# Optimization experiments

Measured on AMD Instinct MI355X. Metric: run time of the kernel, lower is better.

Reference implementation:

```python
import jax, jax.numpy as jnp
import numpy as np

N_NODES = 50000
N_EDGES = 800000
DIMS = [128, 128, 128, 64]  # in, hid1, hid2, out
EPS = 1e-12


def setup_inputs() -> dict:
    key = jax.random.key(0)
    ks = jax.random.split(key, 32)
    inp = {
        "x": jax.random.normal(ks[0], (N_NODES, DIMS[0]), dtype=jnp.float32),
        "edge_src": jax.random.randint(ks[1], (N_EDGES,), 0, N_NODES),
        "edge_dst": jax.random.randint(ks[2], (N_EDGES,), 0, N_NODES),
    }
    k = 3
    for l in range(3):
        din, dout = DIMS[l], DIMS[l + 1]
        s_in = 1.0 / np.sqrt(din)
        inp[f"Wp{l+1}"] = jax.random.uniform(ks[k], (din, din), jnp.float32, -s_in, s_in); k += 1
        inp[f"bp{l+1}"] = jax.random.uniform(ks[k], (din,), jnp.float32, -s_in, s_in); k += 1
        inp[f"Ws{l+1}"] = jax.random.uniform(ks[k], (din, dout), jnp.float32, -s_in, s_in); k += 1
        inp[f"Wn{l+1}"] = jax.random.uniform(ks[k], (din, dout), jnp.float32, -s_in, s_in); k += 1
        inp[f"b{l+1}"] = jnp.zeros((dout,), jnp.float32); k += 1
    return inp


def _sage_pool_layer(x, src, dst, Wp, bp, Ws, Wn, b):
    # per-edge: relu(fc_pool(x_src)); [E, din]
    m = jax.nn.relu(x[src] @ Wp + bp)
    # max-pool over in-neighbors of each dst node; [N, din]
    pooled = jax.ops.segment_max(m, dst, num_segments=x.shape[0])
    deg = jax.ops.segment_sum(jnp.ones((dst.shape[0],), x.dtype), dst,
                              num_segments=x.shape[0])
    pooled = jnp.where(deg[:, None] > 0, pooled, 0.0)  # zero-degree -> 0 (DGL)
    return x @ Ws + pooled @ Wn + b


def _l2norm_relu(h):
    n = jnp.sqrt(jnp.sum(h * h, axis=1, keepdims=True))
    return jax.nn.relu(h / jnp.maximum(n, EPS))


def reference(x, edge_src, edge_dst,
              Wp1, bp1, Ws1, Wn1, b1,
              Wp2, bp2, Ws2, Wn2, b2,
              Wp3, bp3, Ws3, Wn3, b3):
    h = _l2norm_relu(_sage_pool_layer(x, edge_src, edge_dst, Wp1, bp1, Ws1, Wn1, b1))
    h = _l2norm_relu(_sage_pool_layer(h, edge_src, edge_dst, Wp2, bp2, Ws2, Wn2, b2))
    h = _l2norm_relu(_sage_pool_layer(h, edge_src, edge_dst, Wp3, bp3, Ws3, Wn3, b3))
    return h
```

## Files before the change

### kernel.cpp

```cpp
#include <hip/hip_runtime.h>
#include <math.h>

#define N_NODES 50000
#define N_EDGES 800000
#define CAP 64
#define RANGES 8
#define NODES_PER_RANGE 6250
#define GEMMB 782
#define CHUNKS (N_EDGES / 256)
#define CPB 8
#define BPR ((CHUNKS + CPB - 1) / CPB)
#define CSRB (BPR * RANGES)
#define LROW 136

typedef __attribute__((ext_vector_type(8))) short short8;
typedef __attribute__((ext_vector_type(4))) float f32x4;

__device__ __forceinline__ unsigned short f2bf(float f) {
    unsigned int u = __float_as_uint(f);
    return (unsigned short)((u + 0x7FFFu + ((u >> 16) & 1u)) >> 16);
}

template <bool F32>
__device__ __forceinline__ short8 loadA(const void* A, int off) {
    short8 r;
    if (F32) {
        const float* p = (const float*)A + off;
        float4 f0 = *(const float4*)p;
        float4 f1 = *(const float4*)(p + 4);
        r[0] = (short)f2bf(f0.x); r[1] = (short)f2bf(f0.y);
        r[2] = (short)f2bf(f0.z); r[3] = (short)f2bf(f0.w);
        r[4] = (short)f2bf(f1.x); r[5] = (short)f2bf(f1.y);
        r[6] = (short)f2bf(f1.z); r[7] = (short)f2bf(f1.w);
    } else {
        r = *(const short8*)((const unsigned short*)A + off);
    }
    return r;
}

__device__ __forceinline__ void issue8(short8 (&v)[8],
    const unsigned short* a0, const unsigned short* a1) {
    asm volatile(
        "global_load_dwordx4 %0, %8, off\n\t"
        "global_load_dwordx4 %1, %8, off offset:16\n\t"
        "global_load_dwordx4 %2, %8, off offset:32\n\t"
        "global_load_dwordx4 %3, %8, off offset:48\n\t"
        "global_load_dwordx4 %4, %9, off\n\t"
        "global_load_dwordx4 %5, %9, off offset:16\n\t"
        "global_load_dwordx4 %6, %9, off offset:32\n\t"
        "global_load_dwordx4 %7, %9, off offset:48"
        : "=&v"(v[0]), "=&v"(v[1]), "=&v"(v[2]), "=&v"(v[3]),
          "=&v"(v[4]), "=&v"(v[5]), "=&v"(v[6]), "=&v"(v[7])
        : "v"(a0), "v"(a1));
}

__device__ __forceinline__ void wait_vm8(short8 (&v)[8]) {
    asm volatile("s_waitcnt vmcnt(8)"
        : "+v"(v[0]), "+v"(v[1]), "+v"(v[2]), "+v"(v[3]),
          "+v"(v[4]), "+v"(v[5]), "+v"(v[6]), "+v"(v[7]) :: "memory");
}

__device__ __forceinline__ void wait_vm0(short8 (&v)[8]) {
    asm volatile("s_waitcnt vmcnt(0)"
        : "+v"(v[0]), "+v"(v[1]), "+v"(v[2]), "+v"(v[3]),
          "+v"(v[4]), "+v"(v[5]), "+v"(v[6]), "+v"(v[7]) :: "memory");
}

__device__ __forceinline__ void consume8(short8 (&p)[4], const short8 (&v)[8]) {
    p[0] = __builtin_elementwise_max(p[0], v[0]);
    p[1] = __builtin_elementwise_max(p[1], v[1]);
    p[2] = __builtin_elementwise_max(p[2], v[2]);
    p[3] = __builtin_elementwise_max(p[3], v[3]);
    p[0] = __builtin_elementwise_max(p[0], v[4]);
    p[1] = __builtin_elementwise_max(p[1], v[5]);
    p[2] = __builtin_elementwise_max(p[2], v[6]);
    p[3] = __builtin_elementwise_max(p[3], v[7]);
}

struct WDescs { const float* W[9]; int N[9]; };

__global__ __launch_bounds__(256) void prep_kernel(
    WDescs wd, unsigned short* __restrict__ Wpk, int* __restrict__ deg)
{
    const int nthr = gridDim.x * 256;
    const int tid = blockIdx.x * 256 + threadIdx.x;
    for (int id = tid; id < 9 * 16384; id += nthr) {
        int mi = id >> 14;
        int loc = id & 16383;
        int N = wd.N[mi];
        if (loc < 128 * N) {
            int c = loc / (N * 32);
            int n = (loc - c * N * 32) >> 5;
            int k = c * 32 + (loc & 31);
            Wpk[mi * 16384 + loc] = f2bf(wd.W[mi][k * N + n]);
        }
    }
    for (int i = tid; i < N_NODES; i += nthr) deg[i] = 0;
}

__global__ __launch_bounds__(256) void mix_kernel(
    const int* __restrict__ esrc, const int* __restrict__ edst,
    int* __restrict__ deg, unsigned short* __restrict__ csr16,
    const float* __restrict__ x, const unsigned short* __restrict__ Wp1,
    const float* __restrict__ bp1, unsigned short* __restrict__ Y)
{
    if (blockIdx.x >= GEMMB) {
        const int b = blockIdx.x - GEMMB;
        const int range = b & (RANGES - 1);
        const int cbase = (b >> 3) * CPB;
        const int lo = range * NODES_PER_RANGE;
        int d[CPB], s[CPB];
        #pragma unroll
        for (int i = 0; i < CPB; ++i) {
            const int c = cbase + i;
            const int e = c * 256 + threadIdx.x;
            const bool ok = (c < CHUNKS);
            d[i] = ok ? edst[e] : -1;
            s[i] = ok ? esrc[e] : 0;
        }
        #pragma unroll
        for (int i = 0; i < CPB; ++i) {
            if ((unsigned)(d[i] - lo) < (unsigned)NODES_PER_RANGE) {
                int r = atomicAdd(&deg[d[i]], 1);
                if (r < CAP) csr16[(d[i] << 6) + r] = (unsigned short)s[i];
            }
        }
        return;
    }
    const int lane = threadIdx.x & 63;
    const int wv = threadIdx.x >> 6;
    const int cl = lane & 15;
    const int quad = lane >> 4;
    const int rowBase = blockIdx.x * 64 + wv * 16;
    const int ar = min(rowBase + cl, N_NODES - 1);
    const int bLane = cl * 32 + quad * 8;

    f32x4 acc[8];
    #pragma unroll
    for (int t = 0; t < 8; ++t) acc[t] = (f32x4){0.f, 0.f, 0.f, 0.f};

    #pragma unroll
    for (int c = 0; c < 4; ++c) {
        short8 af = loadA<true>(x, ar * 128 + c * 32 + quad * 8);
        const unsigned short* Bc = Wp1 + c * 4096 + bLane;
        #pragma unroll
        for (int t = 0; t < 8; ++t) {
            short8 bf = *(const short8*)(Bc + t * 512);
            acc[t] = __builtin_amdgcn_mfma_f32_16x16x32_bf16(af, bf, acc[t], 0, 0, 0);
        }
    }
    const int row0 = rowBase + quad * 4;
    #pragma unroll
    for (int t = 0; t < 8; ++t) {
        float bc = bp1[t * 16 + cl];
        #pragma unroll
        for (int g = 0; g < 4; ++g) {
            int r = row0 + g;
            if (r < N_NODES)
                Y[r * 128 + t * 16 + cl] = f2bf(fmaxf(acc[t][g] + bc, 0.0f));
        }
    }
}

template <bool A0F32, bool LAST>
__global__ __launch_bounds__(256) void fused_kernel(
    const void* __restrict__ A0,
    const unsigned short* __restrict__ Yl,
    const int* __restrict__ deg,
    const unsigned short* __restrict__ csr16,
    const unsigned short* __restrict__ B0, const unsigned short* __restrict__ B1,
    const float* __restrict__ bias,
    unsigned short* __restrict__ outH, float* __restrict__ outF,
    const unsigned short* __restrict__ Bnext, const float* __restrict__ bnext,
    unsigned short* __restrict__ Yout)
{
    constexpr int NT = LAST ? 4 : 8;
    constexpr int N = NT * 16;
    __shared__ unsigned short lds[4][16 * LROW];

    const int lane = threadIdx.x & 63;
    const int wv = threadIdx.x >> 6;
    const int cl = lane & 15;
    const int quad = lane >> 4;
    const int nodeBase = blockIdx.x * 64 + wv * 16;
    unsigned short* plw = &lds[wv][0];

    {
        const int n16 = lane >> 2;
        const int g   = lane & 3;
        const int node = nodeBase + n16;
        const int nodeC = min(node, N_NODES - 1);
        const int myDeg = (node < N_NODES) ? min(deg[node], CAP) : 0;
        const unsigned short* csrn = csr16 + (nodeC << 6);
        const unsigned short* yg = Yl + g * 32;

        short8 p[4];
        p[0] = (short8){0,0,0,0,0,0,0,0};
        p[1] = p[0]; p[2] = p[0]; p[3] = p[0];

        if (myDeg > 0) {
            unsigned int idxw[16];
            *(uint4*)(idxw +  0) = *(const uint4*)(csrn +  0);
            *(uint4*)(idxw +  4) = *(const uint4*)(csrn +  8);
            *(uint4*)(idxw +  8) = *(const uint4*)(csrn + 16);
            *(uint4*)(idxw + 12) = *(const uint4*)(csrn + 24);
            const int s0 = (int)(idxw[0] & 0xFFFFu);

            auto eaddr = [&](int jj) -> const unsigned short* {
                int sj = (jj & 1) ? (int)(idxw[jj >> 1] >> 16)
                                  : (int)(idxw[jj >> 1] & 0xFFFFu);
                sj = (jj < myDeg) ? sj : s0;
                return yg + (sj << 7);
            };

            short8 va[8], vb[8];
            issue8(va, eaddr(0),  eaddr(1));
            issue8(vb, eaddr(2),  eaddr(3));
            wait_vm8(va); consume8(p, va); issue8(va, eaddr(4),  eaddr(5));
            wait_vm8(vb); consume8(p, vb); issue8(vb, eaddr(6),  eaddr(7));
            wait_vm8(va); consume8(p, va); issue8(va, eaddr(8),  eaddr(9));
            wait_vm8(vb); consume8(p, vb); issue8(vb, eaddr(10), eaddr(11));
            wait_vm8(va); consume8(p, va); issue8(va, eaddr(12), eaddr(13));
            wait_vm8(vb); consume8(p, vb); issue8(vb, eaddr(14), eaddr(15));
            if (myDeg > 16) {
                wait_vm8(va); consume8(p, va); issue8(va, eaddr(16), eaddr(17));
                wait_vm8(vb); consume8(p, vb); issue8(vb, eaddr(18), eaddr(19));
                wait_vm8(va); consume8(p, va); issue8(va, eaddr(20), eaddr(21));
                wait_vm8(vb); consume8(p, vb); issue8(vb, eaddr(22), eaddr(23));
                wait_vm8(va); consume8(p, va); issue8(va, eaddr(24), eaddr(25));
                wait_vm8(vb); consume8(p, vb); issue8(vb, eaddr(26), eaddr(27));
                wait_vm8(va); consume8(p, va); issue8(va, eaddr(28), eaddr(29));
                wait_vm8(vb); consume8(p, vb); issue8(vb, eaddr(30), eaddr(31));
            }
            wait_vm8(va); consume8(p, va);
            wait_vm0(vb); consume8(p, vb);

            for (int k = 32; k < myDeg; ++k) {
                const short8* r = (const short8*)(yg + ((int)csrn[k] << 7));
                p[0] = __builtin_elementwise_max(p[0], r[0]);
                p[1] = __builtin_elementwise_max(p[1], r[1]);
                p[2] = __builtin_elementwise_max(p[2], r[2]);
                p[3] = __builtin_elementwise_max(p[3], r[3]);
            }
        }
        unsigned short* pw = plw + n16 * LROW + g * 32;
        *(short8*)(pw)      = p[0];
        *(short8*)(pw + 8)  = p[1];
        *(short8*)(pw + 16) = p[2];
        *(short8*)(pw + 24) = p[3];
    }

    const int ar = min(nodeBase + cl, N_NODES - 1);
    const int aBase = ar * 128 + quad * 8;
    const int fBase = cl * LROW + quad * 8;
    const int bLane = cl * 32 + quad * 8;

    f32x4 acc[NT];
    #pragma unroll
    for (int t = 0; t < NT; ++t) acc[t] = (f32x4){0.f, 0.f, 0.f, 0.f};

    #pragma unroll
    for (int c = 0; c < 4; ++c) {
        short8 a0 = loadA<A0F32>(A0, aBase + c * 32);
        short8 a1 = *(const short8*)(plw + fBase + c * 32);
        const unsigned short* B0c = B0 + c * (N * 32) + bLane;
        const unsigned short* B1c = B1 + c * (N * 32) + bLane;
        #pragma unroll
        for (int t = 0; t < NT; ++t) {
            short8 bf = *(const short8*)(B0c + t * 512);
            acc[t] = __builtin_amdgcn_mfma_f32_16x16x32_bf16(a0, bf, acc[t], 0, 0, 0);
        }
        #pragma unroll
        for (int t = 0; t < NT; ++t) {
            short8 bf = *(const short8*)(B1c + t * 512);
            acc[t] = __builtin_amdgcn_mfma_f32_16x16x32_bf16(a1, bf, acc[t], 0, 0, 0);
        }
    }

    #pragma unroll
    for (int t = 0; t < NT; ++t) {
        float bc = bias[t * 16 + cl];
        #pragma unroll
        for (int g = 0; g < 4; ++g) acc[t][g] += bc;
    }

    float inv[4];
    #pragma unroll
    for (int g = 0; g < 4; ++g) {
        float s = 0.f;
        #pragma unroll
        for (int t = 0; t < NT; ++t) s += acc[t][g] * acc[t][g];
        s += __shfl_xor(s, 1, 64);
        s += __shfl_xor(s, 2, 64);
        s += __shfl_xor(s, 4, 64);
        s += __shfl_xor(s, 8, 64);
        inv[g] = 1.0f / fmaxf(sqrtf(s), 1e-12f);
    }

    const int row0 = nodeBase + quad * 4;

    if (LAST) {
        #pragma unroll
        for (int t = 0; t < NT; ++t)
            #pragma unroll
            for (int g = 0; g < 4; ++g) {
                int r = row0 + g;
                if (r < N_NODES)
                    outF[r * N + t * 16 + cl] = fmaxf(acc[t][g] * inv[g], 0.0f);
            }
        return;
    }

    #pragma unroll
    for (int t = 0; t < NT; ++t)
        #pragma unroll
        for (int g = 0; g < 4; ++g) {
            int r = row0 + g;
            unsigned short h = f2bf(fmaxf(acc[t][g] * inv[g], 0.0f));
            if (r < N_NODES) outH[r * 128 + t * 16 + cl] = h;
            plw[(quad * 4 + g) * LROW + t * 16 + cl] = h;
        }

    f32x4 ya[8];
    #pragma unroll
    for (int t = 0; t < 8; ++t) ya[t] = (f32x4){0.f, 0.f, 0.f, 0.f};
    #pragma unroll
    for (int c = 0; c < 4; ++c) {
        short8 af = *(const short8*)(plw + cl * LROW + c * 32 + quad * 8);
        const unsigned short* Bc = Bnext + c * 4096 + bLane;
        #pragma unroll
        for (int t = 0; t < 8; ++t) {
            short8 bf = *(const short8*)(Bc + t * 512);
            ya[t] = __builtin_amdgcn_mfma_f32_16x16x32_bf16(af, bf, ya[t], 0, 0, 0);
        }
    }
    #pragma unroll
    for (int t = 0; t < 8; ++t) {
        float bc = bnext[t * 16 + cl];
        #pragma unroll
        for (int g = 0; g < 4; ++g) {
            int r = row0 + g;
            if (r < N_NODES)
                Yout[r * 128 + t * 16 + cl] = f2bf(fmaxf(ya[t][g] + bc, 0.0f));
        }
    }
}

extern "C" void kernel_launch(void* const* d_in, const int* in_sizes, int n_in,
                              void* d_out, int out_size, void* d_ws, size_t ws_size,
                              hipStream_t stream) {
    const float* x    = (const float*)d_in[0];
    const int*   esrc = (const int*)d_in[1];
    const int*   edst = (const int*)d_in[2];
    const float* Wp[3], *bp[3], *Ws[3], *Wn[3], *bb[3];
    for (int l = 0; l < 3; ++l) {
        Wp[l] = (const float*)d_in[3 + 5 * l];
        bp[l] = (const float*)d_in[4 + 5 * l];
        Ws[l] = (const float*)d_in[5 + 5 * l];
        Wn[l] = (const float*)d_in[6 + 5 * l];
        bb[l] = (const float*)d_in[7 + 5 * l];
    }

    const int NF = N_NODES * 128;
    unsigned short* YA  = (unsigned short*)d_ws;
    unsigned short* YB  = YA + NF;
    unsigned short* PL  = YB + NF;
    unsigned short* H1  = PL + NF;
    unsigned short* H2  = H1 + NF;
    unsigned short* Wpk = H2 + NF;
    int* deg = (int*)(Wpk + 9 * 16384);
    unsigned short* csr16 = (unsigned short*)(deg + N_NODES);

    auto WH = [&](int i) { return Wpk + i * 16384; };

    WDescs wd;
    wd.W[0] = Wp[0]; wd.N[0] = 128;
    wd.W[1] = Ws[0]; wd.N[1] = 128;
    wd.W[2] = Wn[0]; wd.N[2] = 128;
    wd.W[3] = Wp[1]; wd.N[3] = 128;
    wd.W[4] = Ws[1]; wd.N[4] = 128;
    wd.W[5] = Wn[1]; wd.N[5] = 128;
    wd.W[6] = Wp[2]; wd.N[6] = 128;
    wd.W[7] = Ws[2]; wd.N[7] = 64;
    wd.W[8] = Wn[2]; wd.N[8] = 64;

    prep_kernel<<<576, 256, 0, stream>>>(wd, Wpk, deg);
    mix_kernel<<<GEMMB + CSRB, 256, 0, stream>>>(esrc, edst, deg, csr16,
                                                 x, WH(0), bp[0], YA);
    fused_kernel<true, false><<<GEMMB, 256, 0, stream>>>(
        x, YA, deg, csr16, WH(1), WH(2), bb[0], H1, nullptr, WH(3), bp[1], YB);
    fused_kernel<false, false><<<GEMMB, 256, 0, stream>>>(
        H1, YB, deg, csr16, WH(4), WH(5), bb[1], H2, nullptr, WH(6), bp[2], YA);
    fused_kernel<false, true><<<GEMMB, 256, 0, stream>>>(
        H2, YA, deg, csr16, WH(7), WH(8), bb[2], nullptr, (float*)d_out,
        nullptr, nullptr, nullptr);
}
```

Before: 331.4 us.

## Fuse all stages into one cooperative persistent kernel with grid syncs

Merges the prep, mix and three fused layer kernels into a single cooperative mega kernel that loops over tasks and separates stages with grid-wide barriers, falling back to separate launches when cooperative launch or occupancy is unavailable. This removes per-kernel launch gaps and the tail between stages. In exchange, grid syncs and thread fences cost time, register pressure is shared across all stage code paths, and the mix stage's CSR blocks must now be looped over by the 782 resident blocks.

After: 336.9 us. About the same (+1.7%).

```diff
diff --git a/kernel.cpp b/kernel.cpp
--- a/kernel.cpp
+++ b/kernel.cpp
@@ -1,5 +1,8 @@
 #include <hip/hip_runtime.h>
+#include <hip/hip_cooperative_groups.h>
 #include <math.h>
+
+namespace cg = cooperative_groups;
 
 #define N_NODES 50000
 #define N_EDGES 800000
@@ -79,8 +82,8 @@
 
 struct WDescs { const float* W[9]; int N[9]; };
 
-__global__ __launch_bounds__(256) void prep_kernel(
-    WDescs wd, unsigned short* __restrict__ Wpk, int* __restrict__ deg)
+__device__ __forceinline__ void do_prep(const WDescs& wd,
+    unsigned short* __restrict__ Wpk, int* __restrict__ deg)
 {
     const int nthr = gridDim.x * 256;
     const int tid = blockIdx.x * 256 + threadIdx.x;
@@ -98,14 +101,14 @@
     for (int i = tid; i < N_NODES; i += nthr) deg[i] = 0;
 }
 
-__global__ __launch_bounds__(256) void mix_kernel(
+__device__ __forceinline__ void do_mix(int task,
     const int* __restrict__ esrc, const int* __restrict__ edst,
     int* __restrict__ deg, unsigned short* __restrict__ csr16,
     const float* __restrict__ x, const unsigned short* __restrict__ Wp1,
     const float* __restrict__ bp1, unsigned short* __restrict__ Y)
 {
-    if (blockIdx.x >= GEMMB) {
-        const int b = blockIdx.x - GEMMB;
+    if (task >= GEMMB) {
+        const int b = task - GEMMB;
         const int range = b & (RANGES - 1);
         const int cbase = (b >> 3) * CPB;
         const int lo = range * NODES_PER_RANGE;
@@ -131,7 +134,7 @@
     const int wv = threadIdx.x >> 6;
     const int cl = lane & 15;
     const int quad = lane >> 4;
-    const int rowBase = blockIdx.x * 64 + wv * 16;
+    const int rowBase = task * 64 + wv * 16;
     const int ar = min(rowBase + cl, N_NODES - 1);
     const int bLane = cl * 32 + quad * 8;
 
@@ -163,7 +166,7 @@
 }
 
 template <bool A0F32, bool LAST>
-__global__ __launch_bounds__(256) void fused_kernel(
+__device__ __forceinline__ void do_fused(int task, unsigned short* ldsAll,
     const void* __restrict__ A0,
     const unsigned short* __restrict__ Yl,
     const int* __restrict__ deg,
@@ -176,14 +179,13 @@
 {
     constexpr int NT = LAST ? 4 : 8;
     constexpr int N = NT * 16;
-    __shared__ unsigned short lds[4][16 * LROW];
 
     const int lane = threadIdx.x & 63;
     const int wv = threadIdx.x >> 6;
     const int cl = lane & 15;
     const int quad = lane >> 4;
-    const int nodeBase = blockIdx.x * 64 + wv * 16;
-    unsigned short* plw = &lds[wv][0];
+    const int nodeBase = task * 64 + wv * 16;
+    unsigned short* plw = ldsAll + wv * (16 * LROW);
 
     {
         const int n16 = lane >> 2;
@@ -346,6 +348,81 @@
     }
 }
 
+struct MegaArgs {
+    const float* x;
+    const int* esrc; const int* edst;
+    WDescs wd;
+    unsigned short *YA, *YB, *H1, *H2, *Wpk;
+    int* deg; unsigned short* csr16;
+    const float *bp1, *bp2, *bp3;
+    const float *b1, *b2, *b3;
+    float* outF;
+};
+
+__device__ __forceinline__ void gsync(cg::grid_group& g) {
+    __threadfence();
+    g.sync();
+    __threadfence();
+}
+
+__global__ __launch_bounds__(256) void mega_kernel(MegaArgs a)
+{
+    cg::grid_group grid = cg::this_grid();
+    __shared__ unsigned short lds[4][16 * LROW];
+    unsigned short* ldsAll = &lds[0][0];
+    const int G = gridDim.x;
+    auto WHd = [&](int i) { return a.Wpk + i * 16384; };
+
+    do_prep(a.wd, a.Wpk, a.deg);
+    gsync(grid);
+    for (int t = blockIdx.x; t < GEMMB + CSRB; t += G)
+        do_mix(t, a.esrc, a.edst, a.deg, a.csr16, a.x, WHd(0), a.bp1, a.YA);
+    gsync(grid);
+    for (int t = blockIdx.x; t < GEMMB; t += G)
+        do_fused<true, false>(t, ldsAll, a.x, a.YA, a.deg, a.csr16,
+            WHd(1), WHd(2), a.b1, a.H1, nullptr, WHd(3), a.bp2, a.YB);
+    gsync(grid);
+    for (int t = blockIdx.x; t < GEMMB; t += G)
+        do_fused<false, false>(t, ldsAll, a.H1, a.YB, a.deg, a.csr16,
+            WHd(4), WHd(5), a.b2, a.H2, nullptr, WHd(6), a.bp3, a.YA);
+    gsync(grid);
+    for (int t = blockIdx.x; t < GEMMB; t += G)
+        do_fused<false, true>(t, ldsAll, a.H2, a.YA, a.deg, a.csr16,
+            WHd(7), WHd(8), a.b3, nullptr, a.outF, nullptr, nullptr, nullptr);
+}
+
+__global__ __launch_bounds__(256) void prep_kernel(
+    WDescs wd, unsigned short* __restrict__ Wpk, int* __restrict__ deg)
+{
+    do_prep(wd, Wpk, deg);
+}
+
+__global__ __launch_bounds__(256) void mix_kernel(
+    const int* __restrict__ esrc, const int* __restrict__ edst,
+    int* __restrict__ deg, unsigned short* __restrict__ csr16,
+    const float* __restrict__ x, const unsigned short* __restrict__ Wp1,
+    const float* __restrict__ bp1, unsigned short* __restrict__ Y)
+{
+    do_mix(blockIdx.x, esrc, edst, deg, csr16, x, Wp1, bp1, Y);
+}
+
+template <bool A0F32, bool LAST>
+__global__ __launch_bounds__(256) void fused_kernel(
+    const void* __restrict__ A0,
+    const unsigned short* __restrict__ Yl,
+    const int* __restrict__ deg,
+    const unsigned short* __restrict__ csr16,
+    const unsigned short* __restrict__ B0, const unsigned short* __restrict__ B1,
+    const float* __restrict__ bias,
+    unsigned short* __restrict__ outH, float* __restrict__ outF,
+    const unsigned short* __restrict__ Bnext, const float* __restrict__ bnext,
+    unsigned short* __restrict__ Yout)
+{
+    __shared__ unsigned short lds[4][16 * LROW];
+    do_fused<A0F32, LAST>(blockIdx.x, &lds[0][0], A0, Yl, deg, csr16,
+                          B0, B1, bias, outH, outF, Bnext, bnext, Yout);
+}
+
 extern "C" void kernel_launch(void* const* d_in, const int* in_sizes, int n_in,
                               void* d_out, int out_size, void* d_ws, size_t ws_size,
                               hipStream_t stream) {
@@ -384,6 +461,35 @@
     wd.W[7] = Ws[2]; wd.N[7] = 64;
     wd.W[8] = Wn[2]; wd.N[8] = 64;
 
+    static int s_mega = -1;
+    if (s_mega < 0) {
+        int coop = 0;
+        hipDeviceGetAttribute(&coop, hipDeviceAttributeCooperativeLaunch, 0);
+        int maxB = 0;
+        hipError_t oe = hipOccupancyMaxActiveBlocksPerMultiprocessor(
+            &maxB, mega_kernel, 256, 0);
+        int cus = 0;
+        hipDeviceProp_t prop;
+        if (hipGetDeviceProperties(&prop, 0) == hipSuccess)
+            cus = prop.multiProcessorCount;
+        s_mega = (coop && oe == hipSuccess && maxB * cus >= GEMMB) ? 1 : 0;
+    }
+
+    if (s_mega == 1) {
+        MegaArgs a;
+        a.x = x; a.esrc = esrc; a.edst = edst; a.wd = wd;
+        a.YA = YA; a.YB = YB; a.H1 = H1; a.H2 = H2; a.Wpk = Wpk;
+        a.deg = deg; a.csr16 = csr16;
+        a.bp1 = bp[0]; a.bp2 = bp[1]; a.bp3 = bp[2];
+        a.b1 = bb[0]; a.b2 = bb[1]; a.b3 = bb[2];
+        a.outF = (float*)d_out;
+        void* params[] = { (void*)&a };
+        hipError_t le = hipLaunchCooperativeKernel(
+            mega_kernel, dim3(GEMMB), dim3(256), params, 0u, stream);
+        if (le == hipSuccess) return;
+        s_mega = 0;
+    }
+
     prep_kernel<<<576, 256, 0, stream>>>(wd, Wpk, deg);
     mix_kernel<<<GEMMB + CSRB, 256, 0, stream>>>(esrc, edst, deg, csr16,
                                                  x, WH(0), bp[0], YA);
```

## Merge three fused layer kernels into one persistent kernel with grid barriers

Applied to the files above, without the earlier changes.

Replaces the three separate fused layer launches with a single kernel that runs all three layers and synchronises between them using atomic grid-wide barriers stored in workspace, plus a memset to reset the barrier counters. The aim is to remove kernel launch gaps and tail effects between layers. It relies on all 782 blocks being co-resident (waves_per_eu pinned to 4), otherwise the spin barrier can deadlock. It also adds barrier spin overhead and restricts register allocation.

New measurement: 876.1 us. 164% more time.

```diff
diff --git a/kernel.cpp b/kernel.cpp
--- a/kernel.cpp
+++ b/kernel.cpp
@@ -79,8 +79,8 @@
 
 struct WDescs { const float* W[9]; int N[9]; };
 
-__global__ __launch_bounds__(256) void prep_kernel(
-    WDescs wd, unsigned short* __restrict__ Wpk, int* __restrict__ deg)
+__device__ __forceinline__ void do_prep(const WDescs& wd,
+    unsigned short* __restrict__ Wpk, int* __restrict__ deg)
 {
     const int nthr = gridDim.x * 256;
     const int tid = blockIdx.x * 256 + threadIdx.x;
@@ -98,14 +98,14 @@
     for (int i = tid; i < N_NODES; i += nthr) deg[i] = 0;
 }
 
-__global__ __launch_bounds__(256) void mix_kernel(
+__device__ __forceinline__ void do_mix(int task,
     const int* __restrict__ esrc, const int* __restrict__ edst,
     int* __restrict__ deg, unsigned short* __restrict__ csr16,
     const float* __restrict__ x, const unsigned short* __restrict__ Wp1,
     const float* __restrict__ bp1, unsigned short* __restrict__ Y)
 {
-    if (blockIdx.x >= GEMMB) {
-        const int b = blockIdx.x - GEMMB;
+    if (task >= GEMMB) {
+        const int b = task - GEMMB;
         const int range = b & (RANGES - 1);
         const int cbase = (b >> 3) * CPB;
         const int lo = range * NODES_PER_RANGE;
@@ -131,7 +131,7 @@
     const int wv = threadIdx.x >> 6;
     const int cl = lane & 15;
     const int quad = lane >> 4;
-    const int rowBase = blockIdx.x * 64 + wv * 16;
+    const int rowBase = task * 64 + wv * 16;
     const int ar = min(rowBase + cl, N_NODES - 1);
     const int bLane = cl * 32 + quad * 8;
 
@@ -163,7 +163,7 @@
 }
 
 template <bool A0F32, bool LAST>
-__global__ __launch_bounds__(256) void fused_kernel(
+__device__ __forceinline__ void do_fused(int task, unsigned short* ldsAll,
     const void* __restrict__ A0,
     const unsigned short* __restrict__ Yl,
     const int* __restrict__ deg,
@@ -176,14 +176,13 @@
 {
     constexpr int NT = LAST ? 4 : 8;
     constexpr int N = NT * 16;
-    __shared__ unsigned short lds[4][16 * LROW];
 
     const int lane = threadIdx.x & 63;
     const int wv = threadIdx.x >> 6;
     const int cl = lane & 15;
     const int quad = lane >> 4;
-    const int nodeBase = blockIdx.x * 64 + wv * 16;
-    unsigned short* plw = &lds[wv][0];
+    const int nodeBase = task * 64 + wv * 16;
+    unsigned short* plw = ldsAll + wv * (16 * LROW);
 
     {
         const int n16 = lane >> 2;
@@ -346,6 +345,66 @@
     }
 }
 
+__global__ __launch_bounds__(256) void prep_kernel(
+    WDescs wd, unsigned short* __restrict__ Wpk, int* __restrict__ deg)
+{
+    do_prep(wd, Wpk, deg);
+}
+
+__global__ __launch_bounds__(256) void mix_kernel(
+    const int* __restrict__ esrc, const int* __restrict__ edst,
+    int* __restrict__ deg, unsigned short* __restrict__ csr16,
+    const float* __restrict__ x, const unsigned short* __restrict__ Wp1,
+    const float* __restrict__ bp1, unsigned short* __restrict__ Y)
+{
+    do_mix(blockIdx.x, esrc, edst, deg, csr16, x, Wp1, bp1, Y);
+}
+
+__device__ __forceinline__ void gridbar(int* bar, int nb, int phase) {
+    __syncthreads();
+    if (threadIdx.x == 0) {
+        __threadfence();
+        if (__hip_atomic_fetch_add(&bar[phase], 1, __ATOMIC_RELEASE,
+                                   __HIP_MEMORY_SCOPE_AGENT) == nb - 1) {
+            __hip_atomic_fetch_add(&bar[7], 1, __ATOMIC_RELEASE,
+                                   __HIP_MEMORY_SCOPE_AGENT);
+        } else {
+            while (__hip_atomic_load(&bar[7], __ATOMIC_ACQUIRE,
+                                     __HIP_MEMORY_SCOPE_AGENT) <= phase)
+                __builtin_amdgcn_s_sleep(8);
+        }
+        __threadfence();
+    }
+    __syncthreads();
+}
+
+__global__ __launch_bounds__(256)
+__attribute__((amdgpu_waves_per_eu(4, 4)))
+void mega3_kernel(
+    const float* x, const int* deg, const unsigned short* csr16,
+    const unsigned short* Wpk,
+    unsigned short* YA, unsigned short* YB,
+    unsigned short* H1, unsigned short* H2,
+    int* bar,
+    const float* b1, const float* b2, const float* b3,
+    const float* bp2, const float* bp3,
+    float* outF)
+{
+    __shared__ unsigned short lds[4][16 * LROW];
+    unsigned short* ldsAll = &lds[0][0];
+    const int task = blockIdx.x;
+    auto WHd = [&](int i) { return Wpk + i * 16384; };
+
+    do_fused<true, false>(task, ldsAll, x, YA, deg, csr16,
+        WHd(1), WHd(2), b1, H1, nullptr, WHd(3), bp2, YB);
+    gridbar(bar, gridDim.x, 0);
+    do_fused<false, false>(task, ldsAll, H1, YB, deg, csr16,
+        WHd(4), WHd(5), b2, H2, nullptr, WHd(6), bp3, YA);
+    gridbar(bar, gridDim.x, 1);
+    do_fused<false, true>(task, ldsAll, H2, YA, deg, csr16,
+        WHd(7), WHd(8), b3, nullptr, outF, nullptr, nullptr, nullptr);
+}
+
 extern "C" void kernel_launch(void* const* d_in, const int* in_sizes, int n_in,
                               void* d_out, int out_size, void* d_ws, size_t ws_size,
                               hipStream_t stream) {
@@ -370,6 +429,7 @@
     unsigned short* Wpk = H2 + NF;
     int* deg = (int*)(Wpk + 9 * 16384);
     unsigned short* csr16 = (unsigned short*)(deg + N_NODES);
+    int* bar = (int*)(csr16 + N_NODES * CAP);
 
     auto WH = [&](int i) { return Wpk + i * 16384; };
 
@@ -387,11 +447,8 @@
     prep_kernel<<<576, 256, 0, stream>>>(wd, Wpk, deg);
     mix_kernel<<<GEMMB + CSRB, 256, 0, stream>>>(esrc, edst, deg, csr16,
                                                  x, WH(0), bp[0], YA);
-    fused_kernel<true, false><<<GEMMB, 256, 0, stream>>>(
-        x, YA, deg, csr16, WH(1), WH(2), bb[0], H1, nullptr, WH(3), bp[1], YB);
-    fused_kernel<false, false><<<GEMMB, 256, 0, stream>>>(
-        H1, YB, deg, csr16, WH(4), WH(5), bb[1], H2, nullptr, WH(6), bp[2], YA);
-    fused_kernel<false, true><<<GEMMB, 256, 0, stream>>>(
-        H2, YA, deg, csr16, WH(7), WH(8), bb[2], nullptr, (float*)d_out,
-        nullptr, nullptr, nullptr);
-}
+    hipMemsetAsync(bar, 0, 8 * sizeof(int), stream);
+    mega3_kernel<<<GEMMB, 256, 0, stream>>>(
+        x, deg, csr16, Wpk, YA, YB, H1, H2, bar,
+        bb[0], bb[1], bb[2], bp[1], bp[2], (float*)d_out);
+}
```
